# Optimization experiments

Hardware: AMD Instinct MI355X
Metric: run time of the kernel (lower is better)

Reference implementation:

```python
import jax, jax.numpy as jnp
import numpy as np

DIM = 192
HEADS = 8
EPS = 1e-12  # torch F.normalize eps


def _l2norm(t):
    # normalize over last axis, matching torch.nn.functional.normalize
    n = jnp.sqrt(jnp.sum(t * t, axis=-1, keepdims=True))
    return t / jnp.maximum(n, EPS)


def setup_inputs() -> dict:
    key = jax.random.key(0)
    k1, k2, k3, k4 = jax.random.split(key, 4)
    B, C, H, W = 16, DIM, 128, 128
    s = 1.0 / np.sqrt(C)
    return {
        "x": jax.random.normal(k1, (B, C, H, W), dtype=jnp.float32),
        "w_qkv": jax.random.normal(k2, (C, 3 * C), dtype=jnp.float32) * s,
        "w_proj": jax.random.normal(k3, (C, C), dtype=jnp.float32) * s,
        "b_proj": jax.random.normal(k4, (C,), dtype=jnp.float32) * 0.01,
        "temperature": jnp.ones((HEADS, 1, 1), dtype=jnp.float32),
    }


def reference(x, w_qkv, w_proj, b_proj, temperature):
    B, C, H, W = x.shape
    N = H * W
    h = HEADS
    d = C // h
    # [B,C,H,W] -> [B,N,C]
    xt = x.reshape(B, C, N).transpose(0, 2, 1)
    qkv = (xt @ w_qkv).reshape(B, N, 3, h, d)
    qkv = qkv.transpose(2, 0, 3, 1, 4)           # [3,B,h,N,d]
    q, k, v = qkv[0], qkv[1], qkv[2]
    # transpose to channel-as-token: [B,h,d,N]
    q = _l2norm(q.transpose(0, 1, 3, 2))
    k = _l2norm(k.transpose(0, 1, 3, 2))
    v = v.transpose(0, 1, 3, 2)
    # small channel attention matrix [B,h,d,d]
    attn = jnp.einsum("bhdn,bhen->bhde", q, k) * temperature
    attn = jax.nn.softmax(attn, axis=-1)
    out = jnp.einsum("bhde,bhen->bhdn", attn, v)  # [B,h,d,N]
    out = out.transpose(0, 3, 1, 2).reshape(B, N, C)
    out = out @ w_proj + b_proj
    return out.transpose(0, 2, 1).reshape(B, C, H, W)
```

## Files before the change

### kernel.cpp

```cpp
#include <hip/hip_runtime.h>
#include <hip/hip_bf16.h>
#include <math.h>

#define C_DIM 192
#define NTOK 16384
#define NB 16
#define NH 8
#define HD 24
#define EPSN 1e-12f

typedef float f32x4 __attribute__((ext_vector_type(4)));
typedef __bf16 bf16x4 __attribute__((ext_vector_type(4)));
typedef __bf16 bf16x8 __attribute__((ext_vector_type(8)));

__device__ __forceinline__ f32x4 mfma16(bf16x8 a, bf16x8 b, f32x4 c) {
  return __builtin_amdgcn_mfma_f32_16x16x32_bf16(a, b, c, 0, 0, 0);
}

__device__ __forceinline__ bf16x8 cvt8(const float* __restrict__ p) {
  f32x4 a = *(const f32x4*)p;
  f32x4 b = *(const f32x4*)(p + 4);
  bf16x8 r;
  r[0] = (__bf16)a[0]; r[1] = (__bf16)a[1]; r[2] = (__bf16)a[2]; r[3] = (__bf16)a[3];
  r[4] = (__bf16)b[0]; r[5] = (__bf16)b[1]; r[6] = (__bf16)b[2]; r[7] = (__bf16)b[3];
  return r;
}

__global__ __launch_bounds__(256, 2) void k1_gram(const float* __restrict__ x,
                                                  float* __restrict__ gpart,
                                                  int kc) {
  const int b = blockIdx.y, chunk = blockIdx.x;
  const float* xb = x + (size_t)b * C_DIM * NTOK + (size_t)chunk * kc;
  __shared__ __bf16 xsh[2][C_DIM * 40];
  const int t = threadIdx.x;
  const int lane = t & 63, wid = t >> 6;
  const int lrow = lane & 15, loct = lane >> 4;
  const int r0 = (wid >> 1) * 96, c0 = (wid & 1) * 96;
  f32x4 acc[6][6] = {};
  f32x4 stg[6];

#pragma unroll
  for (int it = 0; it < 6; ++it) {
    int idx = it * 256 + t, r = idx >> 3, c8 = idx & 7;
    stg[it] = *(const f32x4*)(xb + (size_t)r * NTOK + 4 * c8);
  }
#pragma unroll
  for (int it = 0; it < 6; ++it) {
    int idx = it * 256 + t, r = idx >> 3, c8 = idx & 7;
    bf16x4 w;
    w[0] = (__bf16)stg[it][0]; w[1] = (__bf16)stg[it][1];
    w[2] = (__bf16)stg[it][2]; w[3] = (__bf16)stg[it][3];
    *(bf16x4*)(&xsh[0][r * 40 + 4 * c8]) = w;
  }
  __syncthreads();

  for (int ks = 0; ks < kc; ks += 32) {
    const int cur = (ks >> 5) & 1;
    const bool more = (ks + 32) < kc;
    if (more) {
#pragma unroll
      for (int it = 0; it < 6; ++it) {
        int idx = it * 256 + t, r = idx >> 3, c8 = idx & 7;
        stg[it] = *(const f32x4*)(xb + (size_t)r * NTOK + ks + 32 + 4 * c8);
      }
    }
    bf16x8 fa[6];
#pragma unroll
    for (int i = 0; i < 6; ++i)
      fa[i] = *(const bf16x8*)(&xsh[cur][(r0 + 16 * i + lrow) * 40 + 8 * loct]);
#pragma unroll
    for (int j = 0; j < 6; ++j) {
      bf16x8 fb = *(const bf16x8*)(&xsh[cur][(c0 + 16 * j + lrow) * 40 + 8 * loct]);
#pragma unroll
      for (int i = 0; i < 6; ++i) acc[i][j] = mfma16(fa[i], fb, acc[i][j]);
    }
    if (more) {
#pragma unroll
      for (int it = 0; it < 6; ++it) {
        int idx = it * 256 + t, r = idx >> 3, c8 = idx & 7;
        bf16x4 w;
        w[0] = (__bf16)stg[it][0]; w[1] = (__bf16)stg[it][1];
        w[2] = (__bf16)stg[it][2]; w[3] = (__bf16)stg[it][3];
        *(bf16x4*)(&xsh[cur ^ 1][r * 40 + 4 * c8]) = w;
      }
    }
    __syncthreads();
  }
  float* gp = gpart + ((size_t)chunk * NB + b) * C_DIM * C_DIM;
#pragma unroll
  for (int i = 0; i < 6; ++i)
#pragma unroll
    for (int j = 0; j < 6; ++j)
#pragma unroll
      for (int e = 0; e < 4; ++e)
        gp[(size_t)(r0 + 16 * i + 4 * loct + e) * C_DIM + (c0 + 16 * j + lrow)] =
            acc[i][j][e];
}

__global__ __launch_bounds__(256) void k2a_reduce(const float* __restrict__ gpart,
                                                  float* __restrict__ G,
                                                  int nchunk) {
  const size_t total = (size_t)NB * C_DIM * C_DIM;
  size_t e0 = ((size_t)blockIdx.x * 256 + threadIdx.x) * 4;
  f32x4 s = {};
  for (int c = 0; c < nchunk; ++c) s += *(const f32x4*)(gpart + c * total + e0);
  *(f32x4*)(G + e0) = s;
}

__global__ __launch_bounds__(256) void k2b1_t(const float* __restrict__ G,
                                              const float* __restrict__ wqkv,
                                              float* __restrict__ Tt) {
  const int b = blockIdx.y, rb = blockIdx.x;
  const int lane = threadIdx.x & 63, wid = threadIdx.x >> 6;
  const int lrow = lane & 15, loct = lane >> 4;
  const float* Gb = G + (size_t)b * C_DIM * C_DIM;
  const int ddA = rb * 64 + wid * 16 + lrow;
  f32x4 acc[12] = {};
  for (int s = 0; s < 6; ++s) {
    bf16x8 fa;
#pragma unroll
    for (int e = 0; e < 8; ++e)
      fa[e] = (__bf16)wqkv[(size_t)(32 * s + 8 * loct + e) * 576 + ddA];
#pragma unroll
    for (int j = 0; j < 12; ++j) {
      bf16x8 fb = cvt8(Gb + (size_t)(16 * j + lrow) * C_DIM + 32 * s + 8 * loct);
      acc[j] = mfma16(fa, fb, acc[j]);
    }
  }
  float* To = Tt + (size_t)b * 384 * C_DIM;
#pragma unroll
  for (int j = 0; j < 12; ++j)
#pragma unroll
    for (int e = 0; e < 4; ++e)
      To[(size_t)(rb * 64 + wid * 16 + 4 * loct + e) * C_DIM + 16 * j + lrow] =
          acc[j][e];
}

__global__ __launch_bounds__(256) void k2b2_attn(const float* __restrict__ Tt,
                                                 const float* __restrict__ wqkv,
                                                 const float* __restrict__ temp,
                                                 float* __restrict__ Yt) {
  const int b = blockIdx.y, h = blockIdx.x;
  __shared__ float SL[32][33];
  __shared__ float qn2L[HD], kn2L[HD];
  const int t = threadIdx.x;
  const int lane = t & 63, wid = t >> 6;
  const int lrow = lane & 15, loct = lane >> 4;
  const float* Tb = Tt + (size_t)b * 384 * C_DIM;
  const int r = wid >> 1, j = wid & 1;
  f32x4 acc = {};
  for (int s = 0; s < 6; ++s) {
    bf16x8 fa = cvt8(Tb + (size_t)(h * HD + 16 * r + lrow) * C_DIM + 32 * s + 8 * loct);
    bf16x8 fb;
#pragma unroll
    for (int e = 0; e < 8; ++e)
      fb[e] = (__bf16)wqkv[(size_t)(32 * s + 8 * loct + e) * 576 + 192 + h * HD +
                           16 * j + lrow];
    acc = mfma16(fa, fb, acc);
  }
#pragma unroll
  for (int e = 0; e < 4; ++e) {
    int d = 16 * r + 4 * loct + e, ee = 16 * j + lrow;
    if (d < HD && ee < HD) SL[d][ee] = acc[e];
  }
  if (t < 48) {
    const int dd = (t < 24) ? t : t - 24;
    const int row = ((t < 24) ? 0 : 192) + h * HD + dd;
    float s = 0.f;
    for (int c = 0; c < C_DIM; ++c)
      s += Tb[(size_t)row * C_DIM + c] * wqkv[(size_t)c * 576 + row];
    if (t < 24) qn2L[dd] = s; else kn2L[dd] = s;
  }
  __syncthreads();
  if (t < HD) {
    const float tp = temp[h];
    float nq = fmaxf(sqrtf(fmaxf(qn2L[t], 0.f)), EPSN);
    float lg[HD];
    float m = -1e30f;
#pragma unroll
    for (int e = 0; e < HD; ++e) {
      float nk = fmaxf(sqrtf(fmaxf(kn2L[e], 0.f)), EPSN);
      lg[e] = SL[t][e] / (nq * nk) * tp;
      m = fmaxf(m, lg[e]);
    }
    float sum = 0.f;
#pragma unroll
    for (int e = 0; e < HD; ++e) { lg[e] = __expf(lg[e] - m); sum += lg[e]; }
    float inv = 1.f / sum;
#pragma unroll
    for (int e = 0; e < HD; ++e) SL[t][e] = lg[e] * inv;
  }
  __syncthreads();
  if (t < C_DIM) {
    float wv[HD];
#pragma unroll
    for (int e = 0; e < HD; ++e)
      wv[e] = wqkv[(size_t)t * 576 + 384 + h * HD + e];
    float* Yo = Yt + ((size_t)b * C_DIM + t) * C_DIM + h * HD;
#pragma unroll
    for (int d = 0; d < HD; ++d) {
      float y = 0.f;
#pragma unroll
      for (int e = 0; e < HD; ++e) y += SL[d][e] * wv[e];
      Yo[d] = y;
    }
  }
}

__global__ __launch_bounds__(256) void k2c_m(const float* __restrict__ wproj,
                                             const float* __restrict__ Yt,
                                             __bf16* __restrict__ M) {
  const int b = blockIdx.y, rb = blockIdx.x;
  const int lane = threadIdx.x & 63, wid = threadIdx.x >> 6;
  const int lrow = lane & 15, loct = lane >> 4;
  const float* Yb = Yt + (size_t)b * C_DIM * C_DIM;
  const int coA = rb * 64 + wid * 16 + lrow;
  f32x4 acc[12] = {};
  for (int s = 0; s < 6; ++s) {
    bf16x8 fa;
#pragma unroll
    for (int e = 0; e < 8; ++e)
      fa[e] = (__bf16)wproj[(size_t)(32 * s + 8 * loct + e) * C_DIM + coA];
#pragma unroll
    for (int j = 0; j < 12; ++j) {
      bf16x8 fb = cvt8(Yb + (size_t)(16 * j + lrow) * C_DIM + 32 * s + 8 * loct);
      acc[j] = mfma16(fa, fb, acc[j]);
    }
  }
  __bf16* Mo = M + (size_t)b * C_DIM * C_DIM;
#pragma unroll
  for (int j = 0; j < 12; ++j)
#pragma unroll
    for (int e = 0; e < 4; ++e)
      Mo[(size_t)(rb * 64 + wid * 16 + 4 * loct + e) * C_DIM + 16 * j + lrow] =
          (__bf16)acc[j][e];
}

__global__ __launch_bounds__(256, 4) void k3_out(const float* __restrict__ x,
                                                 const __bf16* __restrict__ M,
                                                 const float* __restrict__ bproj,
                                                 float* __restrict__ out) {
  const int nt = blockIdx.x, half = blockIdx.y, b = blockIdx.z;
  const int rbase = half * 96;
  __shared__ __bf16 Ml[96 * C_DIM];
  __shared__ float biasL[96];
  const int t = threadIdx.x;
  const int lane = t & 63, w = t >> 6;
  const int lrow = lane & 15, loct = lane >> 4;

  const __bf16* Mb = M + (size_t)b * C_DIM * C_DIM + (size_t)rbase * C_DIM;
  for (int i = t; i < 96 * 24; i += 256) {
    int row = i / 24, ch = i % 24;
    bf16x8 v = *(const bf16x8*)(Mb + row * C_DIM + ch * 8);
    *(bf16x8*)(Ml + row * C_DIM + ((ch ^ (row & 7)) * 8)) = v;
  }
  if (t < 96) biasL[t] = bproj[rbase + t];
  __syncthreads();

  const float* xb = x + (size_t)b * C_DIM * NTOK;
  float* ob = out + (size_t)b * C_DIM * NTOK;
  const int n0 = nt * 128 + w * 32;

  f32x4 acc[6][2] = {};
  float xs[2][8];
#pragma unroll
  for (int nf = 0; nf < 2; ++nf)
#pragma unroll
    for (int e = 0; e < 8; ++e)
      xs[nf][e] = xb[(size_t)(8 * loct + e) * NTOK + n0 + 16 * nf + lrow];

  for (int s = 0; s < 6; ++s) {
    bf16x8 fb[2];
#pragma unroll
    for (int nf = 0; nf < 2; ++nf)
#pragma unroll
      for (int e = 0; e < 8; ++e)
        fb[nf][e] = (__bf16)xs[nf][e];
    if (s < 5) {
#pragma unroll
      for (int nf = 0; nf < 2; ++nf)
#pragma unroll
        for (int e = 0; e < 8; ++e)
          xs[nf][e] =
              xb[(size_t)(32 * (s + 1) + 8 * loct + e) * NTOK + n0 + 16 * nf + lrow];
    }
#pragma unroll
    for (int tt = 0; tt < 6; ++tt) {
      int rowb = 16 * tt + lrow;
      bf16x8 fa = *(const bf16x8*)(Ml + rowb * C_DIM +
                                   (((4 * s + loct) ^ (rowb & 7)) * 8));
      acc[tt][0] = mfma16(fa, fb[0], acc[tt][0]);
      acc[tt][1] = mfma16(fa, fb[1], acc[tt][1]);
    }
  }

  __syncthreads();
  float* epi_w = (float*)Ml + w * 544;
#pragma unroll
  for (int tt = 0; tt < 6; ++tt) {
#pragma unroll
    for (int nf = 0; nf < 2; ++nf)
#pragma unroll
      for (int e = 0; e < 4; ++e) {
        int rr = 4 * loct + e;
        epi_w[rr * 33 + 16 * nf + lrow] =
            acc[tt][nf][e] + biasL[16 * tt + rr];
      }
#pragma unroll
    for (int h = 0; h < 2; ++h) {
      int rr = 8 * h + 2 * loct + (lrow >> 3);
      f32x4 v = *(const f32x4*)(epi_w + rr * 33 + 4 * (lrow & 7));
      *(f32x4*)(ob + (size_t)(rbase + 16 * tt + rr) * NTOK + n0 + 4 * (lrow & 7)) = v;
    }
  }
}

extern "C" void kernel_launch(void* const* d_in, const int* in_sizes, int n_in,
                              void* d_out, int out_size, void* d_ws, size_t ws_size,
                              hipStream_t stream) {
  const float* x = (const float*)d_in[0];
  const float* wqkv = (const float*)d_in[1];
  const float* wproj = (const float*)d_in[2];
  const float* bproj = (const float*)d_in[3];
  const float* temp = (const float*)d_in[4];
  float* out = (float*)d_out;

  const size_t GSZ = (size_t)NB * C_DIM * C_DIM;
  const size_t TSZ = (size_t)NB * 384 * C_DIM;
  int nchunk = 32;
  while (nchunk > 1 &&
         ((size_t)nchunk * GSZ + GSZ + TSZ + GSZ + GSZ) * 4 > ws_size)
    nchunk >>= 1;
  float* wsf = (float*)d_ws;
  float* gpart = wsf;
  float* G = gpart + (size_t)nchunk * GSZ;
  float* Tt = G + GSZ;
  float* Yt = Tt + TSZ;
  __bf16* M = (__bf16*)(Yt + GSZ);

  k1_gram<<<dim3(nchunk, NB), 256, 0, stream>>>(x, gpart, NTOK / nchunk);
  k2a_reduce<<<dim3(576), 256, 0, stream>>>(gpart, G, nchunk);
  k2b1_t<<<dim3(6, NB), 256, 0, stream>>>(G, wqkv, Tt);
  k2b2_attn<<<dim3(NH, NB), 256, 0, stream>>>(Tt, wqkv, temp, Yt);
  k2c_m<<<dim3(3, NB), 256, 0, stream>>>(wproj, Yt, M);
  k3_out<<<dim3(128, 2, NB), 256, 0, stream>>>(x, M, bproj, out);
}
```

Baseline: 229.0 us.

## Widen k3_out token tile to 64 per wave with vectorized x loads

Each wave in the output projection kernel now covers 64 tokens instead of 32, so every LDS-loaded M fragment feeds four MFMAs instead of two and half as many blocks reload M into shared memory. Activation loads become 16-byte f32x4 vector loads per lane, with a matching permuted token-to-column mapping, and the epilogue is reorganised to stage vectorized rows through LDS. The costs are more accumulator and staging registers, a lowered launch-bounds occupancy target, and half as many blocks in the grid.

Result: no change. 227.3 us (-0.7%).

```diff
diff --git a/kernel.cpp b/kernel.cpp
--- a/kernel.cpp
+++ b/kernel.cpp
@@ -236,7 +236,7 @@
           (__bf16)acc[j][e];
 }
 
-__global__ __launch_bounds__(256, 4) void k3_out(const float* __restrict__ x,
+__global__ __launch_bounds__(256, 3) void k3_out(const float* __restrict__ x,
                                                  const __bf16* __restrict__ M,
                                                  const float* __restrict__ bproj,
                                                  float* __restrict__ out) {
@@ -259,58 +259,57 @@
 
   const float* xb = x + (size_t)b * C_DIM * NTOK;
   float* ob = out + (size_t)b * C_DIM * NTOK;
-  const int n0 = nt * 128 + w * 32;
-
-  f32x4 acc[6][2] = {};
-  float xs[2][8];
-#pragma unroll
-  for (int nf = 0; nf < 2; ++nf)
-#pragma unroll
-    for (int e = 0; e < 8; ++e)
-      xs[nf][e] = xb[(size_t)(8 * loct + e) * NTOK + n0 + 16 * nf + lrow];
+  const int n0 = nt * 256 + w * 64;
+
+  f32x4 acc[6][4] = {};
+  f32x4 xs4[8];
+#pragma unroll
+  for (int e = 0; e < 8; ++e)
+    xs4[e] = *(const f32x4*)(xb + (size_t)(8 * loct + e) * NTOK + n0 + 4 * lrow);
 
   for (int s = 0; s < 6; ++s) {
-    bf16x8 fb[2];
-#pragma unroll
-    for (int nf = 0; nf < 2; ++nf)
+    bf16x8 fb[4];
+#pragma unroll
+    for (int nf = 0; nf < 4; ++nf)
 #pragma unroll
       for (int e = 0; e < 8; ++e)
-        fb[nf][e] = (__bf16)xs[nf][e];
+        fb[nf][e] = (__bf16)xs4[e][nf];
     if (s < 5) {
 #pragma unroll
-      for (int nf = 0; nf < 2; ++nf)
-#pragma unroll
-        for (int e = 0; e < 8; ++e)
-          xs[nf][e] =
-              xb[(size_t)(32 * (s + 1) + 8 * loct + e) * NTOK + n0 + 16 * nf + lrow];
+      for (int e = 0; e < 8; ++e)
+        xs4[e] = *(const f32x4*)(xb + (size_t)(32 * (s + 1) + 8 * loct + e) * NTOK +
+                                 n0 + 4 * lrow);
     }
 #pragma unroll
     for (int tt = 0; tt < 6; ++tt) {
       int rowb = 16 * tt + lrow;
       bf16x8 fa = *(const bf16x8*)(Ml + rowb * C_DIM +
                                    (((4 * s + loct) ^ (rowb & 7)) * 8));
-      acc[tt][0] = mfma16(fa, fb[0], acc[tt][0]);
-      acc[tt][1] = mfma16(fa, fb[1], acc[tt][1]);
-    }
-  }
-
-  __syncthreads();
-  float* epi_w = (float*)Ml + w * 544;
+#pragma unroll
+      for (int nf = 0; nf < 4; ++nf)
+        acc[tt][nf] = mfma16(fa, fb[nf], acc[tt][nf]);
+    }
+  }
+
+  __syncthreads();
+  float* epi_w = (float*)Ml + w * 1088;
 #pragma unroll
   for (int tt = 0; tt < 6; ++tt) {
-#pragma unroll
-    for (int nf = 0; nf < 2; ++nf)
-#pragma unroll
-      for (int e = 0; e < 4; ++e) {
-        int rr = 4 * loct + e;
-        epi_w[rr * 33 + 16 * nf + lrow] =
-            acc[tt][nf][e] + biasL[16 * tt + rr];
-      }
-#pragma unroll
-    for (int h = 0; h < 2; ++h) {
-      int rr = 8 * h + 2 * loct + (lrow >> 3);
-      f32x4 v = *(const f32x4*)(epi_w + rr * 33 + 4 * (lrow & 7));
-      *(f32x4*)(ob + (size_t)(rbase + 16 * tt + rr) * NTOK + n0 + 4 * (lrow & 7)) = v;
+    f32x4 bias4 = *(const f32x4*)(biasL + 16 * tt + 4 * loct);
+#pragma unroll
+    for (int e = 0; e < 4; ++e) {
+      f32x4 v;
+      v[0] = acc[tt][0][e] + bias4[e];
+      v[1] = acc[tt][1][e] + bias4[e];
+      v[2] = acc[tt][2][e] + bias4[e];
+      v[3] = acc[tt][3][e] + bias4[e];
+      *(f32x4*)(epi_w + (4 * loct + e) * 68 + 4 * lrow) = v;
+    }
+#pragma unroll
+    for (int h = 0; h < 4; ++h) {
+      int r = 4 * h + loct;
+      f32x4 v = *(const f32x4*)(epi_w + r * 68 + 4 * lrow);
+      *(f32x4*)(ob + (size_t)(rbase + 16 * tt + r) * NTOK + n0 + 4 * lrow) = v;
     }
   }
 }
@@ -343,5 +342,5 @@
   k2b1_t<<<dim3(6, NB), 256, 0, stream>>>(G, wqkv, Tt);
   k2b2_attn<<<dim3(NH, NB), 256, 0, stream>>>(Tt, wqkv, temp, Yt);
   k2c_m<<<dim3(3, NB), 256, 0, stream>>>(wproj, Yt, M);
-  k3_out<<<dim3(128, 2, NB), 256, 0, stream>>>(x, M, bproj, out);
-}
+  k3_out<<<dim3(NTOK / 256, 2, NB), 256, 0, stream>>>(x, M, bproj, out);
+}
```
